# Performance work log

Measured on AMD Instinct MI355X. Metric: run time of the kernel, lower is better.

Reference implementation:

```python
import jax, jax.numpy as jnp
import numpy as np


def setup_inputs() -> dict:
    key = jax.random.key(0)
    ks = jax.random.split(key, 7)
    B, D, N, R = 256, 5120, 16, 160  # batch, d_inner, d_state, dt_rank
    x = jax.random.normal(ks[0], (B, D), jnp.float32)
    h0 = jax.random.normal(ks[1], (B, D, N), jnp.float32)
    W_x_dt = jax.random.normal(ks[2], (D, R), jnp.float32) * (1.0 / np.sqrt(D))
    W_dt = jax.random.normal(ks[3], (R, D), jnp.float32) * (1.0 / np.sqrt(R))
    b_dt = jax.random.normal(ks[4], (D,), jnp.float32)
    W_BC = jax.random.normal(ks[5], (D, 2 * N), jnp.float32) * (1.0 / np.sqrt(D))
    A_log = jax.random.normal(ks[6], (D, N), jnp.float32)
    return {"x": x, "h0": h0, "W_x_dt": W_x_dt, "W_dt": W_dt,
            "b_dt": b_dt, "W_BC": W_BC, "A_log": A_log}


def reference(x, h0, W_x_dt, W_dt, b_dt, W_BC, A_log):
    # Single-token Mamba selective SSM step (batch dims squeezed: x [B,D], h0 [B,D,N]).
    N = A_log.shape[1]
    # delta_t = softplus(dt_proj(delta_t_proj(x)))  -> [B, D]
    dt = jax.nn.softplus((x @ W_x_dt) @ W_dt + b_dt)
    # BC projection, split into B and C parts -> [B, N] each
    BC = x @ W_BC
    Bm, Cm = BC[:, :N], BC[:, N:]
    A = -jnp.exp(A_log)                              # [D, N]
    delta_A = jnp.exp(A[None, :, :] * dt[:, :, None])   # [B, D, N]
    delta_Bx = (dt * x)[:, :, None] * Bm[:, None, :]     # [B, D, N]
    h = delta_A * h0 + delta_Bx                          # new hidden state
    # y = h @ C (per-batch bmm over state dim) + x residual
    y = jnp.einsum('bdn,bn->bd', h, Cm) + x              # [B, D]
    return y
```

## Files before the change

### kernel.cpp

```cpp
#include <hip/hip_runtime.h>
#include <math.h>

#define BB 256
#define DD 5120
#define NN 16
#define RR 160
#define CT 192
#define NSPLIT 64
#define KSPL 80
#define TMP_ELEMS (BB * CT)
#define NEGA_ELEMS (DD * NN)

__global__ __launch_bounds__(256) void k1_gemm(const float* __restrict__ x,
                                               const float* __restrict__ Wxdt,
                                               const float* __restrict__ Wbc,
                                               float* __restrict__ part) {
    __shared__ float xs[16][68];
    __shared__ float ws[16][64];
    const int tid = threadIdx.x;
    const int tx = tid & 15, ty = tid >> 4;
    const int c0 = blockIdx.x * 64;
    const int b0 = blockIdx.y * 64;
    const int k0 = blockIdx.z * KSPL;
    float acc[4][4] = {};

    for (int kc = 0; kc < KSPL; kc += 16) {
        {
            const int row = tid >> 2;
            const int j4  = (tid & 3) * 4;
            const float4 v = *(const float4*)&x[(size_t)(b0 + row) * DD + k0 + kc + j4];
            xs[j4 + 0][row] = v.x;
            xs[j4 + 1][row] = v.y;
            xs[j4 + 2][row] = v.z;
            xs[j4 + 3][row] = v.w;
        }
        {
            const int r  = tid >> 4;
            const int c4 = (tid & 15) * 4;
            const int kg = k0 + kc + r;
            const int cg = c0 + c4;
            float4 v;
            if (cg < RR) v = *(const float4*)&Wxdt[(size_t)kg * RR + cg];
            else         v = *(const float4*)&Wbc[(size_t)kg * 32 + (cg - RR)];
            *(float4*)&ws[r][c4] = v;
        }
        __syncthreads();
        #pragma unroll
        for (int k = 0; k < 16; ++k) {
            const float4 a4 = *(const float4*)&xs[k][ty * 4];
            const float4 w4 = *(const float4*)&ws[k][tx * 4];
            const float av[4] = {a4.x, a4.y, a4.z, a4.w};
            const float wv[4] = {w4.x, w4.y, w4.z, w4.w};
            #pragma unroll
            for (int u = 0; u < 4; ++u)
                #pragma unroll
                for (int v = 0; v < 4; ++v)
                    acc[u][v] = fmaf(av[u], wv[v], acc[u][v]);
        }
        __syncthreads();
    }

    float* p = part + (size_t)blockIdx.z * TMP_ELEMS;
    #pragma unroll
    for (int u = 0; u < 4; ++u) {
        const int b = b0 + ty * 4 + u;
        *(float4*)&p[b * CT + c0 + tx * 4] =
            make_float4(acc[u][0], acc[u][1], acc[u][2], acc[u][3]);
    }
}

__global__ __launch_bounds__(256) void k_red(const float* __restrict__ part,
                                             const float* __restrict__ Alog,
                                             float* __restrict__ tmp,
                                             float* __restrict__ negA) {
    const int idx = blockIdx.x * 256 + threadIdx.x;
    if (idx < TMP_ELEMS) {
        float s = 0.f;
        #pragma unroll
        for (int z = 0; z < NSPLIT; ++z) s += part[(size_t)z * TMP_ELEMS + idx];
        tmp[idx] = s;
    } else {
        const int j = idx - TMP_ELEMS;
        negA[j] = -__expf(Alog[j]);
    }
}

__global__ __launch_bounds__(256) void k2_dt(const float* __restrict__ tmp,
                                             const float* __restrict__ Wdt,
                                             const float* __restrict__ bdt,
                                             float* __restrict__ dt) {
    __shared__ float ts[32][34];
    __shared__ float ws[32][64];
    const int tid = threadIdx.x;
    const int tx = tid & 15, ty = tid >> 4;
    const int d0 = blockIdx.x * 64;
    const int b0 = blockIdx.y * 32;
    float acc[2][4] = {};

    for (int kc = 0; kc < RR; kc += 32) {
        {
            const int row = tid >> 3;
            const int j4  = (tid & 7) * 4;
            const float4 v = *(const float4*)&tmp[(size_t)(b0 + row) * CT + kc + j4];
            ts[j4 + 0][row] = v.x;
            ts[j4 + 1][row] = v.y;
            ts[j4 + 2][row] = v.z;
            ts[j4 + 3][row] = v.w;
        }
        {
            const int c4 = (tid & 15) * 4;
            const int r0 = tid >> 4;
            #pragma unroll
            for (int rep = 0; rep < 2; ++rep) {
                const int r = r0 + rep * 16;
                *(float4*)&ws[r][c4] = *(const float4*)&Wdt[(size_t)(kc + r) * DD + d0 + c4];
            }
        }
        __syncthreads();
        #pragma unroll
        for (int k = 0; k < 32; ++k) {
            const float a0 = ts[k][ty * 2 + 0];
            const float a1 = ts[k][ty * 2 + 1];
            const float4 w4 = *(const float4*)&ws[k][tx * 4];
            const float wv[4] = {w4.x, w4.y, w4.z, w4.w};
            #pragma unroll
            for (int v = 0; v < 4; ++v) {
                acc[0][v] = fmaf(a0, wv[v], acc[0][v]);
                acc[1][v] = fmaf(a1, wv[v], acc[1][v]);
            }
        }
        __syncthreads();
    }

    const float4 bv = *(const float4*)&bdt[d0 + tx * 4];
    const float bb[4] = {bv.x, bv.y, bv.z, bv.w};
    #pragma unroll
    for (int u = 0; u < 2; ++u) {
        const int b = b0 + ty * 2 + u;
        float o[4];
        #pragma unroll
        for (int v = 0; v < 4; ++v) {
            const float z = acc[u][v] + bb[v];
            o[v] = fmaxf(z, 0.f) + log1pf(__expf(-fabsf(z)));
        }
        *(float4*)&dt[(size_t)b * DD + d0 + tx * 4] = make_float4(o[0], o[1], o[2], o[3]);
    }
}

__global__ __launch_bounds__(256) void k3_ssm(const float* __restrict__ x,
                                              const float* __restrict__ h0,
                                              const float* __restrict__ dt,
                                              const float* __restrict__ tmp,
                                              const float* __restrict__ negA,
                                              float* __restrict__ out) {
    __shared__ float bcS[32];
    const int tid = threadIdx.x;
    const int b   = blockIdx.y;
    const int d2  = blockIdx.x * 512 + tid * 2;
    const size_t base = (size_t)b * DD + d2;

    if (tid < 32) bcS[tid] = tmp[(size_t)b * CT + RR + tid];
    __syncthreads();

    const float2 xe  = *(const float2*)&x[base];
    const float2 dtv = *(const float2*)&dt[base];
    const float* hp = &h0[base * NN];
    float4 ha[4], hb[4];
    #pragma unroll
    for (int i = 0; i < 4; ++i) ha[i] = *(const float4*)&hp[i * 4];
    #pragma unroll
    for (int i = 0; i < 4; ++i) hb[i] = *(const float4*)&hp[NN + i * 4];
    const float* ap = &negA[(size_t)d2 * NN];
    float4 na0[4], na1[4];
    #pragma unroll
    for (int i = 0; i < 4; ++i) na0[i] = *(const float4*)&ap[i * 4];
    #pragma unroll
    for (int i = 0; i < 4; ++i) na1[i] = *(const float4*)&ap[NN + i * 4];

    const float dt0 = dtv.x, dt1 = dtv.y;
    const float dtx0 = dt0 * xe.x;
    const float dtx1 = dt1 * xe.y;

    float bm[NN], cm[NN];
    #pragma unroll
    for (int n = 0; n < NN; ++n) { bm[n] = bcS[n]; cm[n] = bcS[16 + n]; }

    float y0a = xe.x, y0b = 0.f, y1a = xe.y, y1b = 0.f;
    #pragma unroll
    for (int q4 = 0; q4 < 4; ++q4) {
        const float av0[4] = {na0[q4].x, na0[q4].y, na0[q4].z, na0[q4].w};
        const float av1[4] = {na1[q4].x, na1[q4].y, na1[q4].z, na1[q4].w};
        const float hv0[4] = {ha[q4].x, ha[q4].y, ha[q4].z, ha[q4].w};
        const float hv1[4] = {hb[q4].x, hb[q4].y, hb[q4].z, hb[q4].w};
        #pragma unroll
        for (int q = 0; q < 4; ++q) {
            const int n = q4 * 4 + q;
            const float dA0 = __expf(av0[q] * dt0);
            const float h00 = fmaf(dA0, hv0[q], dtx0 * bm[n]);
            const float dA1 = __expf(av1[q] * dt1);
            const float h11 = fmaf(dA1, hv1[q], dtx1 * bm[n]);
            if (n & 1) { y0b = fmaf(h00, cm[n], y0b); y1b = fmaf(h11, cm[n], y1b); }
            else       { y0a = fmaf(h00, cm[n], y0a); y1a = fmaf(h11, cm[n], y1a); }
        }
    }
    *(float2*)&out[base] = make_float2(y0a + y0b, y1a + y1b);
}

extern "C" void kernel_launch(void* const* d_in, const int* in_sizes, int n_in,
                              void* d_out, int out_size, void* d_ws, size_t ws_size,
                              hipStream_t stream) {
    const float* x    = (const float*)d_in[0];
    const float* h0   = (const float*)d_in[1];
    const float* Wxdt = (const float*)d_in[2];
    const float* Wdt  = (const float*)d_in[3];
    const float* bdt  = (const float*)d_in[4];
    const float* Wbc  = (const float*)d_in[5];
    const float* Alog = (const float*)d_in[6];
    float* out = (float*)d_out;

    float* part  = (float*)d_ws;
    float* tmp   = part + (size_t)NSPLIT * TMP_ELEMS;
    float* negA  = tmp + TMP_ELEMS;
    float* dtbuf = negA + NEGA_ELEMS;

    k1_gemm<<<dim3(3, 4, NSPLIT), 256, 0, stream>>>(x, Wxdt, Wbc, part);
    k_red<<<dim3((TMP_ELEMS + NEGA_ELEMS) / 256), 256, 0, stream>>>(part, Alog, tmp, negA);
    k2_dt<<<dim3(DD / 64, BB / 32), 256, 0, stream>>>(tmp, Wdt, bdt, dtbuf);
    k3_ssm<<<dim3(10, BB), 256, 0, stream>>>(x, h0, dtbuf, tmp, negA, out);
}
```

Baseline: 197.3 us.

## Restructure SSM kernel to quad-per-channel layout and compute -exp(A_log) inline

The SSM kernel now assigns four lanes per channel, each handling four state elements, and loops over 16 batches per block. It reduces the partial sums with shuffles and computes -exp(A_log) once per thread in registers, reused across the batch loop, instead of precomputing negA in the reduction kernel and re-reading it for every batch. This removes the negA buffer's write and repeated reads and gives fully coalesced h0 loads. In exchange, dt and x are loaded as scalars by four lanes each, only one in four lanes writes output, and B/C are reloaded from global memory per batch.

```diff
diff --git a/kernel.cpp b/kernel.cpp
--- a/kernel.cpp
+++ b/kernel.cpp
@@ -9,7 +9,6 @@
 #define NSPLIT 64
 #define KSPL 80
 #define TMP_ELEMS (BB * CT)
-#define NEGA_ELEMS (DD * NN)
 
 __global__ __launch_bounds__(256) void k1_gemm(const float* __restrict__ x,
                                                const float* __restrict__ Wxdt,
@@ -70,19 +69,12 @@
 }
 
 __global__ __launch_bounds__(256) void k_red(const float* __restrict__ part,
-                                             const float* __restrict__ Alog,
-                                             float* __restrict__ tmp,
-                                             float* __restrict__ negA) {
+                                             float* __restrict__ tmp) {
     const int idx = blockIdx.x * 256 + threadIdx.x;
-    if (idx < TMP_ELEMS) {
-        float s = 0.f;
-        #pragma unroll
-        for (int z = 0; z < NSPLIT; ++z) s += part[(size_t)z * TMP_ELEMS + idx];
-        tmp[idx] = s;
-    } else {
-        const int j = idx - TMP_ELEMS;
-        negA[j] = -__expf(Alog[j]);
-    }
+    float s = 0.f;
+    #pragma unroll
+    for (int z = 0; z < NSPLIT; ++z) s += part[(size_t)z * TMP_ELEMS + idx];
+    tmp[idx] = s;
 }
 
 __global__ __launch_bounds__(256) void k2_dt(const float* __restrict__ tmp,
@@ -151,59 +143,38 @@
                                               const float* __restrict__ h0,
                                               const float* __restrict__ dt,
                                               const float* __restrict__ tmp,
-                                              const float* __restrict__ negA,
+                                              const float* __restrict__ Alog,
                                               float* __restrict__ out) {
-    __shared__ float bcS[32];
     const int tid = threadIdx.x;
-    const int b   = blockIdx.y;
-    const int d2  = blockIdx.x * 512 + tid * 2;
-    const size_t base = (size_t)b * DD + d2;
-
-    if (tid < 32) bcS[tid] = tmp[(size_t)b * CT + RR + tid];
-    __syncthreads();
-
-    const float2 xe  = *(const float2*)&x[base];
-    const float2 dtv = *(const float2*)&dt[base];
-    const float* hp = &h0[base * NN];
-    float4 ha[4], hb[4];
-    #pragma unroll
-    for (int i = 0; i < 4; ++i) ha[i] = *(const float4*)&hp[i * 4];
-    #pragma unroll
-    for (int i = 0; i < 4; ++i) hb[i] = *(const float4*)&hp[NN + i * 4];
-    const float* ap = &negA[(size_t)d2 * NN];
-    float4 na0[4], na1[4];
-    #pragma unroll
-    for (int i = 0; i < 4; ++i) na0[i] = *(const float4*)&ap[i * 4];
-    #pragma unroll
-    for (int i = 0; i < 4; ++i) na1[i] = *(const float4*)&ap[NN + i * 4];
-
-    const float dt0 = dtv.x, dt1 = dtv.y;
-    const float dtx0 = dt0 * xe.x;
-    const float dtx1 = dt1 * xe.y;
-
-    float bm[NN], cm[NN];
-    #pragma unroll
-    for (int n = 0; n < NN; ++n) { bm[n] = bcS[n]; cm[n] = bcS[16 + n]; }
-
-    float y0a = xe.x, y0b = 0.f, y1a = xe.y, y1b = 0.f;
-    #pragma unroll
-    for (int q4 = 0; q4 < 4; ++q4) {
-        const float av0[4] = {na0[q4].x, na0[q4].y, na0[q4].z, na0[q4].w};
-        const float av1[4] = {na1[q4].x, na1[q4].y, na1[q4].z, na1[q4].w};
-        const float hv0[4] = {ha[q4].x, ha[q4].y, ha[q4].z, ha[q4].w};
-        const float hv1[4] = {hb[q4].x, hb[q4].y, hb[q4].z, hb[q4].w};
-        #pragma unroll
-        for (int q = 0; q < 4; ++q) {
-            const int n = q4 * 4 + q;
-            const float dA0 = __expf(av0[q] * dt0);
-            const float h00 = fmaf(dA0, hv0[q], dtx0 * bm[n]);
-            const float dA1 = __expf(av1[q] * dt1);
-            const float h11 = fmaf(dA1, hv1[q], dtx1 * bm[n]);
-            if (n & 1) { y0b = fmaf(h00, cm[n], y0b); y1b = fmaf(h11, cm[n], y1b); }
-            else       { y0a = fmaf(h00, cm[n], y0a); y1a = fmaf(h11, cm[n], y1a); }
-        }
-    }
-    *(float2*)&out[base] = make_float2(y0a + y0b, y1a + y1b);
+    const int q = tid >> 2;
+    const int l = tid & 3;
+    const int d = blockIdx.x * 64 + q;
+    const int b0 = blockIdx.y * 16;
+
+    const float4 av = *(const float4*)&Alog[(size_t)d * NN + l * 4];
+    const float na[4] = {-__expf(av.x), -__expf(av.y), -__expf(av.z), -__expf(av.w)};
+
+    #pragma unroll 4
+    for (int bi = 0; bi < 16; ++bi) {
+        const int b = b0 + bi;
+        const size_t bd = (size_t)b * DD + d;
+        const float4 h4 = *(const float4*)&h0[bd * NN + l * 4];
+        const float dtv = dt[bd];
+        const float xv  = x[bd];
+        const float4 bm4 = *(const float4*)&tmp[(size_t)b * CT + RR + l * 4];
+        const float4 cm4 = *(const float4*)&tmp[(size_t)b * CT + RR + 16 + l * 4];
+        const float dtx = dtv * xv;
+
+        float p0, p1;
+        p0 = fmaf(__expf(na[0] * dtv), h4.x, dtx * bm4.x) * cm4.x;
+        p1 = fmaf(__expf(na[1] * dtv), h4.y, dtx * bm4.y) * cm4.y;
+        p0 = fmaf(fmaf(__expf(na[2] * dtv), h4.z, dtx * bm4.z), cm4.z, p0);
+        p1 = fmaf(fmaf(__expf(na[3] * dtv), h4.w, dtx * bm4.w), cm4.w, p1);
+        float p = p0 + p1;
+        p += __shfl_xor(p, 1);
+        p += __shfl_xor(p, 2);
+        if (l == 0) out[bd] = xv + p;
+    }
 }
 
 extern "C" void kernel_launch(void* const* d_in, const int* in_sizes, int n_in,
@@ -220,11 +191,10 @@
 
     float* part  = (float*)d_ws;
     float* tmp   = part + (size_t)NSPLIT * TMP_ELEMS;
-    float* negA  = tmp + TMP_ELEMS;
-    float* dtbuf = negA + NEGA_ELEMS;
+    float* dtbuf = tmp + TMP_ELEMS;
 
     k1_gemm<<<dim3(3, 4, NSPLIT), 256, 0, stream>>>(x, Wxdt, Wbc, part);
-    k_red<<<dim3((TMP_ELEMS + NEGA_ELEMS) / 256), 256, 0, stream>>>(part, Alog, tmp, negA);
+    k_red<<<dim3(TMP_ELEMS / 256), 256, 0, stream>>>(part, tmp);
     k2_dt<<<dim3(DD / 64, BB / 32), 256, 0, stream>>>(tmp, Wdt, bdt, dtbuf);
-    k3_ssm<<<dim3(10, BB), 256, 0, stream>>>(x, h0, dtbuf, tmp, negA, out);
-}
+    k3_ssm<<<dim3(DD / 64, BB / 16), 256, 0, stream>>>(x, h0, dtbuf, tmp, Alog, out);
+}
```

After: 188.2 us. -4.6%, faster.
